# Optimization experiments

Hardware: AMD Instinct MI355X
Metric: run time of the kernel (lower is better)

Reference implementation:

```python
import jax, jax.numpy as jnp
import numpy as np

NUM_EMBEDDINGS = 8192
EMBEDDING_DIM = 256
COMMITMENT_COST = 0.25


def setup_inputs() -> dict:
    key = jax.random.key(0)
    k1, k2 = jax.random.split(key)
    inputs = jax.random.normal(k1, (64, 512, EMBEDDING_DIM), dtype=jnp.float32)
    # nn.Embedding weight initialized uniform(-0.1, 0.1)
    emb_w = jax.random.uniform(k2, (NUM_EMBEDDINGS, EMBEDDING_DIM), dtype=jnp.float32,
                               minval=-0.1, maxval=0.1)
    return {"inputs": inputs, "emb_w": emb_w}


def reference(inputs, emb_w):
    x = jnp.clip(inputs, -1.0, 1.0)
    flat = x.reshape(-1, EMBEDDING_DIM)                      # [N, D]
    distances = (jnp.sum(flat * flat, axis=1, keepdims=True)
                 + jnp.sum(emb_w * emb_w, axis=1)
                 - 2.0 * jnp.einsum('nd,kd->nk', flat, emb_w))
    encoding_indices = jnp.argmin(distances, axis=1)         # [N]
    quantized = emb_w[encoding_indices].reshape(x.shape)     # [B, T, D]
    # loss = mse(stop_grad(q), x) + beta * mse(q, stop_grad(x))
    loss = (jnp.mean((jax.lax.stop_gradient(quantized) - x) ** 2)
            + COMMITMENT_COST * jnp.mean((quantized - jax.lax.stop_gradient(x)) ** 2))
    # straight-through estimator
    quantized_st = x + jax.lax.stop_gradient(quantized - x)
    return (quantized_st, loss)
```

## Files before the change

### kernel.cpp

```cpp
#include <hip/hip_runtime.h>


#define D        256
#define KCODES   8192
#define NROWS    32768
#define MB       64
#define SLOTS    128
#define THREADS  512
#define CAP      32
#define MARGIN   0.03f
#define BIAS     32.0f
#define NOUT     8388608

typedef _Float16 h8_t __attribute__((ext_vector_type(8)));
typedef float    f4_t __attribute__((ext_vector_type(4)));

__device__ __forceinline__ float clipf(float v) { return fminf(1.0f, fmaxf(-1.0f, v)); }

#define DPP_ROR(x, n) __int_as_float(__builtin_amdgcn_update_dpp( \
    0, __float_as_int(x), 0x120 + (n), 0xF, 0xF, true))
__device__ __forceinline__ float maxrow16(float x) {
  x = fmaxf(x, DPP_ROR(x, 1));
  x = fmaxf(x, DPP_ROR(x, 2));
  x = fmaxf(x, DPP_ROR(x, 4));
  x = fmaxf(x, DPP_ROR(x, 8));
  return x;
}

__global__ void vq_packsetup(const float* __restrict__ emb, _Float16* __restrict__ femb,
                             float* __restrict__ senp, float* __restrict__ ekkb,
                             float* __restrict__ lossacc) {
  const int t = blockIdx.x;
  if (t == 0 && threadIdx.x == 0) lossacc[0] = 0.0f;
  {
    int g = t * 256 + threadIdx.x;
    int ch = g >> 9, u = g & 511;
    int kc = u >> 6, ln = u & 63;
    int code = ch * 16 + (ln & 15);
    int k0 = kc * 32 + (ln >> 4) * 8;
    const float* sp = emb + (size_t)code * D + k0;
    f4_t v0 = *(const f4_t*)sp, v1 = *(const f4_t*)(sp + 4);
    h8_t h;
    h[0] = (_Float16)v0[0]; h[1] = (_Float16)v0[1];
    h[2] = (_Float16)v0[2]; h[3] = (_Float16)v0[3];
    h[4] = (_Float16)v1[0]; h[5] = (_Float16)v1[1];
    h[6] = (_Float16)v1[2]; h[7] = (_Float16)v1[3];
    *(h8_t*)(femb + (size_t)g * 8) = h;
  }
  if (t < 256) {
    const int lane = threadIdx.x & 63;
    const int w    = threadIdx.x >> 6;
    const int jdx  = lane & 15, hf = jdx >> 3, jj = jdx & 7;
    #pragma unroll
    for (int cc = 0; cc < 2; ++cc) {
      int k = t * 32 + w * 8 + cc * 4 + (lane >> 4);
      const float* base = emb + (size_t)k * D + hf * 128 + jj;
      float v = base[0];
      float r = v * v;
      #pragma unroll
      for (int m = 1; m < 16; ++m) { v = base[8 * m]; r += v * v; }
      r += __shfl_xor(r, 1, 64);
      r += __shfl_xor(r, 2, 64);
      r += __shfl_xor(r, 4, 64);
      r += __shfl_xor(r, 8, 64);
      if (jdx == 0) { senp[k] = r; ekkb[k] = 0.5f * r - BIAS; }
    }
  }
}

__global__ void __launch_bounds__(THREADS, 4)
vq_score(const float* __restrict__ xin, const _Float16* __restrict__ femb,
         const float* __restrict__ ekkb, int* __restrict__ gcnt,
         unsigned short* __restrict__ gcand) {
  __shared__ alignas(16) char Astage[32768];
  __shared__ int rowmaxI[MB];
  __shared__ int cnt[MB];
  __shared__ int ncnt[MB];
  __shared__ unsigned short cand[MB][CAP];
  __shared__ float scoref[MB][CAP];

  const int tid  = threadIdx.x;
  const int lane = tid & 63;
  const int wid  = tid >> 6;
  const int l15  = lane & 15;
  const int quad = lane >> 4;
  const int rw   = wid >> 2;
  const int cq   = wid & 3;
  const int r0   = blockIdx.x * MB;

  for (int i = tid; i < MB; i += THREADS) { rowmaxI[i] = 0; cnt[i] = 0; ncnt[i] = 0; }

  #pragma unroll
  for (int j = 0; j < 4; ++j) {
    int c = j * THREADS + tid;
    int ms = c >> 9, kc = (c >> 6) & 7, ln = c & 63;
    int row = ms * 16 + (ln & 15);
    int k0 = kc * 32 + (ln >> 4) * 8;
    const float* ap = xin + (size_t)(r0 + row) * D + k0;
    f4_t v0 = *(const f4_t*)ap, v1 = *(const f4_t*)(ap + 4);
    h8_t h;
    h[0] = (_Float16)clipf(v0[0]); h[1] = (_Float16)clipf(v0[1]);
    h[2] = (_Float16)clipf(v0[2]); h[3] = (_Float16)clipf(v0[3]);
    h[4] = (_Float16)clipf(v1[0]); h[5] = (_Float16)clipf(v1[1]);
    h[6] = (_Float16)clipf(v1[2]); h[7] = (_Float16)clipf(v1[3]);
    *(h8_t*)(Astage + (size_t)c * 16) = h;
  }
  __syncthreads();

  h8_t afrag[2][8];
  #pragma unroll
  for (int m = 0; m < 2; ++m)
    #pragma unroll
    for (int kc = 0; kc < 8; ++kc)
      afrag[m][kc] = *(const h8_t*)(Astage +
          (size_t)(((rw * 2 + m) * 512 + kc * 64 + lane) * 16));

  float Gm[2];
  Gm[0] = -1e30f; Gm[1] = -1e30f;

  h8_t bufA[4], bufB[4]; float ekcur;
  {
    const _Float16* bb = femb + (size_t)cq * 4096 + lane * 8;
    #pragma unroll
    for (int kc = 0; kc < 4; ++kc) bufA[kc] = *(const h8_t*)(bb + kc * 512);
    #pragma unroll
    for (int kc = 0; kc < 4; ++kc) bufB[kc] = *(const h8_t*)(bb + (4 + kc) * 512);
    ekcur = ekkb[cq * 16 + l15];
  }

  for (int s = 0; s < SLOTS; ++s) {
    const int sn = (s + 1 < SLOTS) ? s + 1 : s;
    const _Float16* bbn = femb + (size_t)(sn * 4 + cq) * 4096 + lane * 8;

    f4_t acc[2];
    #pragma unroll
    for (int m = 0; m < 2; ++m) { f4_t z = {0.f, 0.f, 0.f, 0.f}; acc[m] = z; }

    #pragma unroll
    for (int kc = 0; kc < 4; ++kc)
      #pragma unroll
      for (int m = 0; m < 2; ++m)
        acc[m] = __builtin_amdgcn_mfma_f32_16x16x32_f16(afrag[m][kc], bufA[kc], acc[m], 0, 0, 0);
    #pragma unroll
    for (int kc = 0; kc < 4; ++kc) bufA[kc] = *(const h8_t*)(bbn + kc * 512);

    #pragma unroll
    for (int kc = 0; kc < 4; ++kc)
      #pragma unroll
      for (int m = 0; m < 2; ++m)
        acc[m] = __builtin_amdgcn_mfma_f32_16x16x32_f16(afrag[m][4 + kc], bufB[kc], acc[m], 0, 0, 0);
    #pragma unroll
    for (int kc = 0; kc < 4; ++kc) bufB[kc] = *(const h8_t*)(bbn + (4 + kc) * 512);

    float eknext = ekkb[(sn * 4 + cq) * 16 + l15];

    const int ch = s * 4 + cq;
    #pragma unroll
    for (int m = 0; m < 2; ++m) {
      float ts[4];
      #pragma unroll
      for (int r = 0; r < 4; ++r) ts[r] = acc[m][r] - ekcur;
      float tmx = fmaxf(fmaxf(ts[0], ts[1]), fmaxf(ts[2], ts[3]));
      if (__any(tmx > Gm[m])) {
        float cmin = 1e30f;
        #pragma unroll
        for (int r = 0; r < 4; ++r) {
          int row_ = rw * 32 + m * 16 + quad * 4 + r;
          float mm = maxrow16(ts[r]);
          if (l15 == 0) atomicMax(&rowmaxI[row_], __float_as_int(mm));
          float cut = __int_as_float(rowmaxI[row_]) - MARGIN;
          cmin = fminf(cmin, cut);
          if (ts[r] >= cut) {
            int sidx = atomicAdd(&cnt[row_], 1);
            if (sidx < CAP) {
              cand[row_][sidx]   = (unsigned short)(ch * 16 + l15);
              scoref[row_][sidx] = ts[r];
            }
          }
        }
        Gm[m] = cmin;
      }
    }
    ekcur = eknext;
    if ((s & 31) == 31) __syncthreads();
  }
  __syncthreads();

  {
    const int row = tid >> 3, j = tid & 7;
    int valid = cnt[row]; if (valid > CAP) valid = CAP;
    const float cut = __int_as_float(rowmaxI[row]) - MARGIN;
    for (int jj = j; jj < valid; jj += 8) {
      if (scoref[row][jj] >= cut) {
        int ns = atomicAdd(&ncnt[row], 1);
        gcand[(size_t)(r0 + row) * CAP + ns] = cand[row][jj];
      }
    }
  }
  __syncthreads();
  if (tid < MB) gcnt[r0 + tid] = ncnt[tid];
}

__global__ void __launch_bounds__(512)
vq_rescore(const float* __restrict__ xin, const float* __restrict__ emb,
           const float* __restrict__ senp, const int* __restrict__ gcnt,
           const unsigned short* __restrict__ gcand, float* __restrict__ out,
           float* __restrict__ lossacc) {
  __shared__ float xrow[8][D];
  __shared__ float rpart[8][16];
  __shared__ float blksum;
  const int tid  = threadIdx.x;
  const int lane = tid & 63;
  const int wid  = tid >> 6;
  const int g    = lane >> 3;
  const int e    = lane & 7;
  const int r0   = blockIdx.x * 64;
  if (tid == 0) blksum = 0.0f;
  __syncthreads();

  const int lane4 = lane * 4;
  float lacc = 0.0f;

  int ncs[8], k0s[8];
  #pragma unroll
  for (int rr = 0; rr < 8; ++rr) {
    int row = r0 + wid + rr * 8;
    ncs[rr] = gcnt[row];
    k0s[rr] = gcand[(size_t)row * CAP];
  }

  f4_t evs[8], xvs[8];
  #pragma unroll
  for (int rr = 0; rr < 8; ++rr) {
    if (ncs[rr] == 1) {
      int row = r0 + wid + rr * 8;
      xvs[rr] = *(const f4_t*)(xin + (size_t)row * D + lane4);
      evs[rr] = *(const f4_t*)(emb + (size_t)k0s[rr] * D + lane4);
    }
  }
  #pragma unroll
  for (int rr = 0; rr < 8; ++rr) {
    if (ncs[rr] == 1) {
      int row = r0 + wid + rr * 8;
      f4_t xv = xvs[rr];
      xv[0] = clipf(xv[0]); xv[1] = clipf(xv[1]);
      xv[2] = clipf(xv[2]); xv[3] = clipf(xv[3]);
      f4_t ev = evs[rr];
      *(f4_t*)(out + (size_t)row * D + lane4) = ev;
      #pragma unroll
      for (int i = 0; i < 4; ++i) { float df = ev[i] - xv[i]; lacc += df * df; }
    }
  }

  for (int rr = 0; rr < 8; ++rr) {
    if (ncs[rr] != 1) {
      const int row = wid + rr * 8;
      f4_t xv = *(const f4_t*)(xin + (size_t)(r0 + row) * D + lane4);
      xv[0] = clipf(xv[0]); xv[1] = clipf(xv[1]);
      xv[2] = clipf(xv[2]); xv[3] = clipf(xv[3]);
      *(f4_t*)&xrow[wid][lane4] = xv;
      __builtin_amdgcn_wave_barrier();
      if (lane < 16) {
        const int hf = lane >> 3, jj = lane & 7;
        const float* base = &xrow[wid][hf * 128 + jj];
        float v = base[0];
        float rs = v * v;
        #pragma unroll
        for (int m = 1; m < 16; ++m) { v = base[8 * m]; rs += v * v; }
        rpart[wid][lane] = rs;
      }
      __builtin_amdgcn_wave_barrier();
      float p[16];
      #pragma unroll
      for (int j = 0; j < 16; ++j) p[j] = rpart[wid][j];
      float h0 = ((p[0] + p[1]) + (p[2] + p[3])) + ((p[4] + p[5]) + (p[6] + p[7]));
      float h1 = ((p[8] + p[9]) + (p[10] + p[11])) + ((p[12] + p[13]) + (p[14] + p[15]));
      float sx = h0 + h1;

      f4_t xo[8];
      #pragma unroll
      for (int u = 0; u < 8; ++u) xo[u] = *(const f4_t*)&xrow[wid][e * 32 + u * 4];

      const int nc = ncs[rr];
      const unsigned short* cl = gcand + (size_t)(r0 + row) * CAP;
      float bd = INFINITY; int bk = 0x7fffffff;
      for (int bi = 0; bi < (nc + 7) >> 3; ++bi) {
        int ci = bi * 8 + g;
        bool valid = ci < nc;
        int k = valid ? cl[ci] : 0;
        const float* ep = emb + (size_t)k * D + e * 32;
        double dd = 0.0;
        #pragma unroll
        for (int u = 0; u < 8; ++u) {
          f4_t ev = *(const f4_t*)(ep + u * 4);
          dd += (double)xo[u][0] * (double)ev[0] + (double)xo[u][1] * (double)ev[1]
              + (double)xo[u][2] * (double)ev[2] + (double)xo[u][3] * (double)ev[3];
        }
        dd += __shfl_xor(dd, 1, 64);
        dd += __shfl_xor(dd, 2, 64);
        dd += __shfl_xor(dd, 4, 64);
        float T1 = sx + senp[k];
        float T2 = (float)(2.0 * dd);
        float d  = valid ? (T1 - T2) : INFINITY;
        int   kk = valid ? k : 0x7fffffff;
        if (d < bd || (d == bd && kk < bk)) { bd = d; bk = kk; }
      }
      #pragma unroll
      for (int off = 8; off < 64; off <<= 1) {
        float od = __shfl_xor(bd, off, 64);
        int   ok = __shfl_xor(bk, off, 64);
        if (od < bd || (od == bd && ok < bk)) { bd = od; bk = ok; }
      }

      f4_t ev = *(const f4_t*)(emb + (size_t)bk * D + lane4);
      *(f4_t*)(out + (size_t)(r0 + row) * D + lane4) = ev;
      #pragma unroll
      for (int i = 0; i < 4; ++i) { float df = ev[i] - xv[i]; lacc += df * df; }
    }
  }

  #pragma unroll
  for (int off = 1; off < 64; off <<= 1) lacc += __shfl_xor(lacc, off, 64);
  if (lane == 0) atomicAdd(&blksum, lacc);
  __syncthreads();
  if (tid == 0) atomicAdd(lossacc, blksum);
}

__global__ void vq_fin(const float* __restrict__ lossacc, float* __restrict__ out) {
  out[NOUT] = 1.25f * lossacc[0] / 8388608.0f;
}

extern "C" void kernel_launch(void* const* d_in, const int* in_sizes, int n_in,
                              void* d_out, int out_size, void* d_ws, size_t ws_size,
                              hipStream_t stream) {
  const float* xin = (const float*)d_in[0];
  const float* emb = (const float*)d_in[1];
  float* out = (float*)d_out;
  _Float16* femb = (_Float16*)d_ws;
  float* F       = (float*)d_ws + 1048576;
  float* senp    = F;
  float* ekkb    = F + 8192;
  float* lossacc = F + 16384;
  int*   gcnt    = (int*)(F + 16640);
  unsigned short* gcand = (unsigned short*)(F + 16640 + 32768);
  vq_packsetup<<<dim3(1024), dim3(256), 0, stream>>>(emb, femb, senp, ekkb, lossacc);
  vq_score<<<dim3(NROWS / MB), dim3(THREADS), 0, stream>>>(xin, femb, ekkb, gcnt, gcand);
  vq_rescore<<<dim3(NROWS / 64), dim3(512), 0, stream>>>(xin, emb, senp, gcnt, gcand, out, lossacc);
  vq_fin<<<dim3(1), dim3(1), 0, stream>>>(lossacc, out);
}
```

Before: 286.1 us.

## Track per-lane running row maxima and share them periodically instead of per-hit atomics

The candidate-selection loop keeps a per-lane running maximum for each row in registers and compares scores against it on every step. Shared-memory atomicMax and a block barrier now run only every 8 slots, replacing the atomic-and-reload that ran each time any lane beat the threshold. Candidate capacity doubles, and rows that overflow it are flagged with -1 so the rescore kernel falls back to a full exact scan of all codes. The local thresholds are looser, so more candidates get written, and the barrier now runs every 8 slots instead of every 32.

New measurement: 316.1 us. 1.1x slower.

```diff
diff --git a/kernel.cpp b/kernel.cpp
--- a/kernel.cpp
+++ b/kernel.cpp
@@ -7,7 +7,7 @@
 #define MB       64
 #define SLOTS    128
 #define THREADS  512
-#define CAP      32
+#define CAP      64
 #define MARGIN   0.03f
 #define BIAS     32.0f
 #define NOUT     8388608
@@ -115,8 +115,11 @@
       afrag[m][kc] = *(const h8_t*)(Astage +
           (size_t)(((rw * 2 + m) * 512 + kc * 64 + lane) * 16));
 
-  float Gm[2];
-  Gm[0] = -1e30f; Gm[1] = -1e30f;
+  float rml[2][4];
+  #pragma unroll
+  for (int m = 0; m < 2; ++m)
+    #pragma unroll
+    for (int r = 0; r < 4; ++r) rml[m][r] = -1e30f;
 
   h8_t bufA[4], bufB[4]; float ekcur;
   {
@@ -160,45 +163,60 @@
       float ts[4];
       #pragma unroll
       for (int r = 0; r < 4; ++r) ts[r] = acc[m][r] - ekcur;
-      float tmx = fmaxf(fmaxf(ts[0], ts[1]), fmaxf(ts[2], ts[3]));
-      if (__any(tmx > Gm[m])) {
-        float cmin = 1e30f;
+      #pragma unroll
+      for (int r = 0; r < 4; ++r) {
+        float mm = maxrow16(ts[r]);
+        rml[m][r] = fmaxf(rml[m][r], mm);
+        if (ts[r] >= rml[m][r] - MARGIN) {
+          int row_ = rw * 32 + m * 16 + quad * 4 + r;
+          int sidx = atomicAdd(&cnt[row_], 1);
+          if (sidx < CAP) {
+            cand[row_][sidx]   = (unsigned short)(ch * 16 + l15);
+            scoref[row_][sidx] = ts[r];
+          }
+        }
+      }
+    }
+    ekcur = eknext;
+
+    if ((s & 7) == 7) {
+      #pragma unroll
+      for (int m = 0; m < 2; ++m)
         #pragma unroll
         for (int r = 0; r < 4; ++r) {
           int row_ = rw * 32 + m * 16 + quad * 4 + r;
-          float mm = maxrow16(ts[r]);
-          if (l15 == 0) atomicMax(&rowmaxI[row_], __float_as_int(mm));
-          float cut = __int_as_float(rowmaxI[row_]) - MARGIN;
-          cmin = fminf(cmin, cut);
-          if (ts[r] >= cut) {
-            int sidx = atomicAdd(&cnt[row_], 1);
-            if (sidx < CAP) {
-              cand[row_][sidx]   = (unsigned short)(ch * 16 + l15);
-              scoref[row_][sidx] = ts[r];
-            }
-          }
-        }
-        Gm[m] = cmin;
-      }
-    }
-    ekcur = eknext;
-    if ((s & 31) == 31) __syncthreads();
+          if (l15 == 0) atomicMax(&rowmaxI[row_], __float_as_int(rml[m][r]));
+        }
+      __syncthreads();
+      #pragma unroll
+      for (int m = 0; m < 2; ++m)
+        #pragma unroll
+        for (int r = 0; r < 4; ++r) {
+          int row_ = rw * 32 + m * 16 + quad * 4 + r;
+          rml[m][r] = fmaxf(rml[m][r], __int_as_float(rowmaxI[row_]));
+        }
+    }
   }
   __syncthreads();
 
   {
     const int row = tid >> 3, j = tid & 7;
-    int valid = cnt[row]; if (valid > CAP) valid = CAP;
-    const float cut = __int_as_float(rowmaxI[row]) - MARGIN;
-    for (int jj = j; jj < valid; jj += 8) {
-      if (scoref[row][jj] >= cut) {
-        int ns = atomicAdd(&ncnt[row], 1);
-        gcand[(size_t)(r0 + row) * CAP + ns] = cand[row][jj];
-      }
-    }
-  }
-  __syncthreads();
-  if (tid < MB) gcnt[r0 + tid] = ncnt[tid];
+    const int c = cnt[row];
+    if (c <= CAP) {
+      const float cut = __int_as_float(rowmaxI[row]) - MARGIN;
+      for (int jj = j; jj < c; jj += 8) {
+        if (scoref[row][jj] >= cut) {
+          int ns = atomicAdd(&ncnt[row], 1);
+          gcand[(size_t)(r0 + row) * CAP + ns] = cand[row][jj];
+        }
+      }
+    }
+  }
+  __syncthreads();
+  if (tid < MB) {
+    int c = cnt[tid];
+    gcnt[r0 + tid] = (c > CAP) ? -1 : ncnt[tid];
+  }
 }
 
 __global__ void __launch_bounds__(512)
@@ -235,7 +253,7 @@
     if (ncs[rr] == 1) {
       int row = r0 + wid + rr * 8;
       xvs[rr] = *(const f4_t*)(xin + (size_t)row * D + lane4);
-      evs[rr] = *(const f4_t*)(emb + (size_t)k0s[rr] * D + lane4);
+      evs[rr] = *(const f4_t*)(emb + (size_t)(k0s[rr] & (KCODES - 1)) * D + lane4);
     }
   }
   #pragma unroll
@@ -282,12 +300,14 @@
       for (int u = 0; u < 8; ++u) xo[u] = *(const f4_t*)&xrow[wid][e * 32 + u * 4];
 
       const int nc = ncs[rr];
+      const bool fullscan = (nc < 0);
+      const int niter = fullscan ? (KCODES >> 3) : ((nc + 7) >> 3);
       const unsigned short* cl = gcand + (size_t)(r0 + row) * CAP;
       float bd = INFINITY; int bk = 0x7fffffff;
-      for (int bi = 0; bi < (nc + 7) >> 3; ++bi) {
+      for (int bi = 0; bi < niter; ++bi) {
         int ci = bi * 8 + g;
-        bool valid = ci < nc;
-        int k = valid ? cl[ci] : 0;
+        bool valid = fullscan ? true : (ci < nc);
+        int k = fullscan ? ci : (valid ? (int)cl[ci] : 0);
         const float* ep = emb + (size_t)k * D + e * 32;
         double dd = 0.0;
         #pragma unroll
@@ -311,6 +331,7 @@
         int   ok = __shfl_xor(bk, off, 64);
         if (od < bd || (od == bd && ok < bk)) { bd = od; bk = ok; }
       }
+      bk &= (KCODES - 1);
 
       f4_t ev = *(const f4_t*)(emb + (size_t)bk * D + lane4);
       *(f4_t*)(out + (size_t)(r0 + row) * D + lane4) = ev;
```
